# Performance work log

Hardware: AMD Instinct MI355X
Metric: run time of the kernel (lower is better)

Reference implementation:

```python
import jax, jax.numpy as jnp
import numpy as np

N_QUBITS = 11
N_LAYERS = 4
N_FEATURES = 8
N_SAMPLES = 16
MEAS_QUBITS = (0, 1, 2, 3)
DIM = 2 ** N_QUBITS


def _cnot_matrix(control, target, n):
    # Faithful to get_single_CNOT_matrix: qubit 0 is the MOST significant bit
    # (bin(i).zfill(n) indexing). Column i maps to row with target bit flipped
    # when control bit is 1.
    idx = np.arange(2 ** n)
    ctrl = (idx >> (n - 1 - control)) & 1
    rows = np.where(ctrl == 1, idx ^ (1 << (n - 1 - target)), idx)
    u = np.zeros((2 ** n, 2 ** n), np.float32)
    u[rows, idx] = 1.0
    return jnp.asarray(u, jnp.complex64)


def _get_angles(X, weights, biases):
    # X: (B, F) -> angles (B, L, Q, 3), tiling features with repetition
    B, F = X.shape
    n_angles = N_QUBITS * N_LAYERS * 3
    reps = n_angles // F + 1
    Xe = jnp.tile(X, (1, reps))[:, :n_angles].reshape(B, N_LAYERS, N_QUBITS, 3)
    return Xe * weights[None] + biases[None]


def _single_qubit_unitaries(ang):
    # ang: (B, Q, 3) = (phi, theta, omega)  ->  (B, Q, 2, 2) complex Rot gates
    phi, theta, omega = ang[..., 0], ang[..., 1], ang[..., 2]
    ct = jnp.cos(theta / 2)
    st = jnp.sin(theta / 2)
    po = (phi + omega) / 2
    pm = (phi - omega) / 2
    m00 = jnp.exp(-1j * po) * ct
    m01 = -jnp.exp(1j * pm) * st
    m10 = jnp.exp(-1j * pm) * st
    m11 = jnp.exp(1j * po) * ct
    M = jnp.stack([m00, m01, m10, m11], axis=-1)
    return M.reshape(ang.shape[0], ang.shape[1], 2, 2).astype(jnp.complex64)


def _system_unitary(M):
    # Sequential Kronecker product over qubits (qubit 0 = leftmost factor),
    # identical math to the source's einsum-based kron: (B, 2^n, 2^n).
    B = M.shape[0]
    U = M[:, 0]
    for q in range(1, N_QUBITS):
        d = U.shape[1]
        U = (U[:, :, None, :, None] * M[:, q][:, None, :, None, :]).reshape(B, d * 2, d * 2)
    return U


def setup_inputs() -> dict:
    key = jax.random.key(0)
    k1, k2, k3 = jax.random.split(key, 3)
    X = jax.random.normal(k1, (N_SAMPLES, N_FEATURES), jnp.float32)
    weights = jax.random.uniform(k2, (N_LAYERS, N_QUBITS, 3), jnp.float32)
    biases = jax.random.uniform(k3, (N_LAYERS, N_QUBITS, 3), jnp.float32)
    return {"X": X, "weights": weights, "biases": biases}


def reference(X, weights, biases):
    B = X.shape[0]
    angles = _get_angles(X, weights, biases)  # (B, L, Q, 3)
    state = jnp.zeros((B, DIM), jnp.complex64).at[:, 0].set(1.0)
    ring = [(i, i + 1) for i in range(N_QUBITS - 1)] + [(N_QUBITS - 1, 0)]
    cnots = [_cnot_matrix(c, t, N_QUBITS) for c, t in ring]
    for l in range(N_LAYERS):
        U = _system_unitary(_single_qubit_unitaries(angles[:, l]))  # (B, D, D)
        state = jnp.einsum('aij,aj->ai', U, state)
        for Uc in cnots:
            state = jnp.einsum('ij,aj->ai', Uc, state)
    probs = jnp.abs(state) ** 2  # (B, D) float32
    idx = jnp.arange(DIM)
    outs = [jnp.sum(probs * (1.0 - 2.0 * ((idx >> (N_QUBITS - 1 - q)) & 1)).astype(probs.dtype), axis=1)
            for q in MEAS_QUBITS]
    return jnp.stack(outs, axis=1)  # (B, n_meas)
```

## Files before the change

### kernel.cpp

```cpp
#include <hip/hip_runtime.h>

#define NQ 11
#define NL 4
#define NF 8
#define DIM 2048
#define NGATES (NL * NQ)

__host__ __device__ constexpr int ring_perm(int y) {
    int z = y ^ ((y & 1) << 10);
    for (int k = 10; k >= 1; --k)
        z ^= ((z >> (11 - k)) & 1) << (10 - k);
    return z;
}

__device__ __forceinline__ int swz(int i) { return i ^ ((i >> 5) & 31); }

__device__ __forceinline__ void wave_sync() { __builtin_amdgcn_wave_barrier(); }

__device__ __forceinline__ float2 cmul(float2 a, float2 b) {
    return make_float2(a.x * b.x - a.y * b.y, a.x * b.y + a.y * b.x);
}

__device__ __forceinline__ void rot_pair(float2& a, float2& c,
                                         const float4 M0, const float4 M1) {
    float2 na, nc;
    na.x = M0.x * a.x - M0.y * a.y + M0.z * c.x - M0.w * c.y;
    na.y = M0.x * a.y + M0.y * a.x + M0.z * c.y + M0.w * c.x;
    nc.x = M1.x * a.x - M1.y * a.y + M1.z * c.x - M1.w * c.y;
    nc.y = M1.x * a.y + M1.y * a.x + M1.z * c.y + M1.w * c.x;
    a = na; c = nc;
}

template<int P2, int P1, int P0, bool PERM>
__device__ __forceinline__ void group3(const float2* __restrict__ src,
                                       float2* __restrict__ dst,
                                       const float (*gm)[8], int g, int base) {
    constexpr int E2 = 1 << P2, E1 = 1 << P1, E0 = 1 << P0;
    constexpr int K2 = PERM ? ring_perm(1 << P2) : (1 << P2);
    constexpr int K1 = PERM ? ring_perm(1 << P1) : (1 << P1);
    constexpr int K0 = PERM ? ring_perm(1 << P0) : (1 << P0);

    const float4* mA = (const float4*)gm[g];
    const float4* mB = (const float4*)gm[g + 1];
    const float4* mC = (const float4*)gm[g + 2];
    const float4 A0 = mA[0], A1 = mA[1];
    const float4 B0 = mB[0], B1 = mB[1];
    const float4 C0 = mC[0], C1 = mC[1];

    const int rb = PERM ? ring_perm(base) : base;
    float2 s[8];
#pragma unroll
    for (int k = 0; k < 8; ++k) {
        const int idx = rb ^ ((k & 4) ? K2 : 0) ^ ((k & 2) ? K1 : 0) ^ ((k & 1) ? K0 : 0);
        s[k] = src[swz(idx)];
    }
    rot_pair(s[0], s[4], A0, A1); rot_pair(s[1], s[5], A0, A1);
    rot_pair(s[2], s[6], A0, A1); rot_pair(s[3], s[7], A0, A1);
    rot_pair(s[0], s[2], B0, B1); rot_pair(s[1], s[3], B0, B1);
    rot_pair(s[4], s[6], B0, B1); rot_pair(s[5], s[7], B0, B1);
    rot_pair(s[0], s[1], C0, C1); rot_pair(s[2], s[3], C0, C1);
    rot_pair(s[4], s[5], C0, C1); rot_pair(s[6], s[7], C0, C1);
#pragma unroll
    for (int k = 0; k < 8; ++k) {
        const int a = base | ((k & 4) ? E2 : 0) | ((k & 2) ? E1 : 0) | ((k & 1) ? E0 : 0);
        dst[swz(a)] = s[k];
    }
}

__device__ __forceinline__ void group2q(float2* buf, const float (*gm)[8],
                                        int g, int t) {
    const float4* mB = (const float4*)gm[g];
    const float4* mC = (const float4*)gm[g + 1];
    const float4 B0 = mB[0], B1 = mB[1];
    const float4 C0 = mC[0], C1 = mC[1];
#pragma unroll
    for (int j = 0; j < 2; ++j) {
        const int base = (t << 3) | (j << 2);
        float2 s[4];
#pragma unroll
        for (int k = 0; k < 4; ++k) s[k] = buf[swz(base | k)];
        rot_pair(s[0], s[2], B0, B1); rot_pair(s[1], s[3], B0, B1);
        rot_pair(s[0], s[1], C0, C1); rot_pair(s[2], s[3], C0, C1);
#pragma unroll
        for (int k = 0; k < 4; ++k) buf[swz(base | k)] = s[k];
    }
}

__global__ __launch_bounds__(256)
void qsim_kernel(const float* __restrict__ X, const float* __restrict__ W,
                 const float* __restrict__ Bi, float* __restrict__ out)
{
    __shared__ float2 bufA[DIM];
    __shared__ float2 bufB[DIM];
    __shared__ __align__(16) float gm[NGATES][8];
    __shared__ float sc[3 * NGATES][2];
    __shared__ float red[4][4];

    const int b = blockIdx.x;
    const int t = threadIdx.x;

    if (t < 3 * NGATES) {
        const int g = t / 3, c = t - 3 * g;
        const int base = g * 3;
        const float x0 = X[b * NF + ((base + 0) & 7)];
        const float x1 = X[b * NF + ((base + 1) & 7)];
        const float x2 = X[b * NF + ((base + 2) & 7)];
        const float phi   = x0 * W[base + 0] + Bi[base + 0];
        const float theta = x1 * W[base + 1] + Bi[base + 1];
        const float omega = x2 * W[base + 2] + Bi[base + 2];
        const float arg = (c == 0) ? 0.5f * theta
                        : (c == 1) ? 0.5f * (phi + omega)
                                   : 0.5f * (phi - omega);
        float s_, c_; sincosf(arg, &s_, &c_);
        sc[t][0] = s_; sc[t][1] = c_;
    }
    __syncthreads();
    if (t < NGATES) {
        const float sh  = sc[3 * t][0],     ch  = sc[3 * t][1];
        const float spo = sc[3 * t + 1][0], cpo = sc[3 * t + 1][1];
        const float spm = sc[3 * t + 2][0], cpm = sc[3 * t + 2][1];
        gm[t][0] =  cpo * ch;  gm[t][1] = -spo * ch;
        gm[t][2] = -cpm * sh;  gm[t][3] = -spm * sh;
        gm[t][4] =  cpm * sh;  gm[t][5] = -spm * sh;
        gm[t][6] =  cpo * ch;  gm[t][7] =  spo * ch;
    }
    __syncthreads();

    float2* S = bufA;
    float2* T = bufB;

    {
        float2 c0[11], c1[11];
#pragma unroll
        for (int q = 0; q < 11; ++q) {
            c0[q] = make_float2(gm[q][0], gm[q][1]);
            c1[q] = make_float2(gm[q][4], gm[q][5]);
        }
        float2 P = ((t >> 0) & 1) ? c1[10] : c0[10];
#pragma unroll
        for (int bbit = 1; bbit < 8; ++bbit)
            P = cmul(P, ((t >> bbit) & 1) ? c1[10 - bbit] : c0[10 - bbit]);
        float2 t2[4];
        t2[0] = cmul(c0[1], c0[0]);
        t2[1] = cmul(c1[1], c0[0]);
        t2[2] = cmul(c0[1], c1[0]);
        t2[3] = cmul(c1[1], c1[0]);
#pragma unroll
        for (int k = 0; k < 8; ++k) {
            const float2 h = cmul((k & 1) ? c1[2] : c0[2], t2[k >> 1]);
            S[swz(t + 256 * k)] = cmul(P, h);
        }
    }
    __syncthreads();

    for (int l = 1; l < NL; ++l) {
        group3<10, 9, 8, true>(S, T, gm, l * NQ + 0, t); { float2* x = S; S = T; T = x; }
        __syncthreads();
        const int base765 = ((t >> 5) << 8) | (t & 31);
        const int base432 = ((t >> 2) << 5) | (t & 3);
        group3<7, 6, 5, false>(S, S, gm, l * NQ + 3, base765);  wave_sync();
        group3<4, 3, 2, false>(S, S, gm, l * NQ + 6, base432);  wave_sync();
        group2q(S, gm, l * NQ + 9, t);
        __syncthreads();
    }

    const int rp_t = ring_perm(t);
    float v[4] = {0.f, 0.f, 0.f, 0.f};
#pragma unroll
    for (int k = 0; k < 8; ++k) {
        const int src = rp_t ^ ((k & 4) ? ring_perm(1 << 10) : 0)
                             ^ ((k & 2) ? ring_perm(1 << 9)  : 0)
                             ^ ((k & 1) ? ring_perm(1 << 8)  : 0);
        const float2 a = S[swz(src)];
        const float p = a.x * a.x + a.y * a.y;
        v[0] += (k & 4) ? -p : p;
        v[1] += (k & 2) ? -p : p;
        v[2] += (k & 1) ? -p : p;
        v[3] += (t & 128) ? -p : p;
    }
#pragma unroll
    for (int q = 0; q < 4; ++q)
#pragma unroll
        for (int off = 32; off >= 1; off >>= 1)
            v[q] += __shfl_down(v[q], off, 64);
    if ((t & 63) == 0) {
#pragma unroll
        for (int q = 0; q < 4; ++q) red[t >> 6][q] = v[q];
    }
    __syncthreads();
    if (t < 4) {
        out[b * 4 + t] = red[0][t] + red[1][t] + red[2][t] + red[3][t];
    }
}

extern "C" void kernel_launch(void* const* d_in, const int* in_sizes, int n_in,
                              void* d_out, int out_size, void* d_ws, size_t ws_size,
                              hipStream_t stream) {
    const float* X  = (const float*)d_in[0];
    const float* W  = (const float*)d_in[1];
    const float* Bi = (const float*)d_in[2];
    float* out = (float*)d_out;
    qsim_kernel<<<16, 256, 0, stream>>>(X, W, Bi, out);
}
```

Measured before the change: 66.44 us.

## Fuse final gate layer with measurement and use per-wave gate setup sync

The last layer's final two rotations are fused with the PauliZ measurement: each thread computes probabilities in registers and derives the parity signs through the ring CNOT permutation, which removes one block barrier and a shared-memory pass. Gate-matrix setup is restructured so each wave handles whole gates, letting a wave barrier replace a block barrier. The layer loop is also unrolled. This relies on correct parity-mask algebra for the CNOT ring.

Result: faster. 65.05 us (median of 2 runs) (-2.1%).

```diff
diff --git a/kernel.cpp b/kernel.cpp
--- a/kernel.cpp
+++ b/kernel.cpp
@@ -86,6 +86,40 @@
     }
 }
 
+__device__ __forceinline__ void group2q_meas(const float2* __restrict__ buf,
+                                             const float (*gm)[8], int g, int t,
+                                             float v[4]) {
+    const float4* mB = (const float4*)gm[g];
+    const float4* mC = (const float4*)gm[g + 1];
+    const float4 B0 = mB[0], B1 = mB[1];
+    const float4 C0 = mC[0], C1 = mC[1];
+    const int tb = t << 3;
+    const int p0 = __popc(tb & 0x3FF) & 1;
+    const int p1 = __popc(tb & 0x600) & 1;
+    const int p2 = __popc(tb & 0x700) & 1;
+    const int p3 = __popc(tb & 0x780) & 1;
+    float Psum = 0.f, Aalt = 0.f;
+#pragma unroll
+    for (int j = 0; j < 2; ++j) {
+        const int base = tb | (j << 2);
+        float2 s[4];
+#pragma unroll
+        for (int k = 0; k < 4; ++k) s[k] = buf[swz(base | k)];
+        rot_pair(s[0], s[2], B0, B1); rot_pair(s[1], s[3], B0, B1);
+        rot_pair(s[0], s[1], C0, C1); rot_pair(s[2], s[3], C0, C1);
+#pragma unroll
+        for (int k = 0; k < 4; ++k) {
+            const float p = s[k].x * s[k].x + s[k].y * s[k].y;
+            Psum += p;
+            Aalt += (__popc((j << 2) | k) & 1) ? -p : p;
+        }
+    }
+    v[0] = p0 ? -Aalt : Aalt;
+    v[1] = p1 ? -Psum : Psum;
+    v[2] = p2 ? -Psum : Psum;
+    v[3] = p3 ? -Psum : Psum;
+}
+
 __global__ __launch_bounds__(256)
 void qsim_kernel(const float* __restrict__ X, const float* __restrict__ W,
                  const float* __restrict__ Bi, float* __restrict__ out)
@@ -93,36 +127,40 @@
     __shared__ float2 bufA[DIM];
     __shared__ float2 bufB[DIM];
     __shared__ __align__(16) float gm[NGATES][8];
-    __shared__ float sc[3 * NGATES][2];
+    __shared__ float sc[192][2];
     __shared__ float red[4][4];
 
     const int b = blockIdx.x;
     const int t = threadIdx.x;
 
-    if (t < 3 * NGATES) {
-        const int g = t / 3, c = t - 3 * g;
-        const int base = g * 3;
-        const float x0 = X[b * NF + ((base + 0) & 7)];
-        const float x1 = X[b * NF + ((base + 1) & 7)];
-        const float x2 = X[b * NF + ((base + 2) & 7)];
-        const float phi   = x0 * W[base + 0] + Bi[base + 0];
-        const float theta = x1 * W[base + 1] + Bi[base + 1];
-        const float omega = x2 * W[base + 2] + Bi[base + 2];
-        const float arg = (c == 0) ? 0.5f * theta
-                        : (c == 1) ? 0.5f * (phi + omega)
-                                   : 0.5f * (phi - omega);
-        float s_, c_; sincosf(arg, &s_, &c_);
-        sc[t][0] = s_; sc[t][1] = c_;
-    }
-    __syncthreads();
-    if (t < NGATES) {
-        const float sh  = sc[3 * t][0],     ch  = sc[3 * t][1];
-        const float spo = sc[3 * t + 1][0], cpo = sc[3 * t + 1][1];
-        const float spm = sc[3 * t + 2][0], cpm = sc[3 * t + 2][1];
-        gm[t][0] =  cpo * ch;  gm[t][1] = -spo * ch;
-        gm[t][2] = -cpm * sh;  gm[t][3] = -spm * sh;
-        gm[t][4] =  cpm * sh;  gm[t][5] = -spm * sh;
-        gm[t][6] =  cpo * ch;  gm[t][7] =  spo * ch;
+    {
+        const int sl = t & 63;
+        const int g = 21 * (t >> 6) + sl / 3;
+        const int c = sl % 3;
+        if (sl < 63 && g < NGATES) {
+            const int base = g * 3;
+            const float x0 = X[b * NF + ((base + 0) & 7)];
+            const float x1 = X[b * NF + ((base + 1) & 7)];
+            const float x2 = X[b * NF + ((base + 2) & 7)];
+            const float phi   = x0 * W[base + 0] + Bi[base + 0];
+            const float theta = x1 * W[base + 1] + Bi[base + 1];
+            const float omega = x2 * W[base + 2] + Bi[base + 2];
+            const float arg = (c == 0) ? 0.5f * theta
+                            : (c == 1) ? 0.5f * (phi + omega)
+                                       : 0.5f * (phi - omega);
+            float s_, c_; sincosf(arg, &s_, &c_);
+            sc[t][0] = s_; sc[t][1] = c_;
+        }
+        wave_sync();
+        if (sl < 63 && g < NGATES && c == 0) {
+            const float sh  = sc[t][0],     ch  = sc[t][1];
+            const float spo = sc[t + 1][0], cpo = sc[t + 1][1];
+            const float spm = sc[t + 2][0], cpm = sc[t + 2][1];
+            gm[g][0] =  cpo * ch;  gm[g][1] = -spo * ch;
+            gm[g][2] = -cpm * sh;  gm[g][3] = -spm * sh;
+            gm[g][4] =  cpm * sh;  gm[g][5] = -spm * sh;
+            gm[g][6] =  cpo * ch;  gm[g][7] =  spo * ch;
+        }
     }
     __syncthreads();
 
@@ -153,6 +191,7 @@
     }
     __syncthreads();
 
+#pragma unroll
     for (int l = 1; l < NL; ++l) {
         group3<10, 9, 8, true>(S, T, gm, l * NQ + 0, t); { float2* x = S; S = T; T = x; }
         __syncthreads();
@@ -160,24 +199,15 @@
         const int base432 = ((t >> 2) << 5) | (t & 3);
         group3<7, 6, 5, false>(S, S, gm, l * NQ + 3, base765);  wave_sync();
         group3<4, 3, 2, false>(S, S, gm, l * NQ + 6, base432);  wave_sync();
-        group2q(S, gm, l * NQ + 9, t);
-        __syncthreads();
-    }
-
-    const int rp_t = ring_perm(t);
-    float v[4] = {0.f, 0.f, 0.f, 0.f};
-#pragma unroll
-    for (int k = 0; k < 8; ++k) {
-        const int src = rp_t ^ ((k & 4) ? ring_perm(1 << 10) : 0)
-                             ^ ((k & 2) ? ring_perm(1 << 9)  : 0)
-                             ^ ((k & 1) ? ring_perm(1 << 8)  : 0);
-        const float2 a = S[swz(src)];
-        const float p = a.x * a.x + a.y * a.y;
-        v[0] += (k & 4) ? -p : p;
-        v[1] += (k & 2) ? -p : p;
-        v[2] += (k & 1) ? -p : p;
-        v[3] += (t & 128) ? -p : p;
-    }
+        if (l < NL - 1) {
+            group2q(S, gm, l * NQ + 9, t);
+            __syncthreads();
+        }
+    }
+
+    float v[4];
+    group2q_meas(S, gm, (NL - 1) * NQ + 9, t, v);
+
 #pragma unroll
     for (int q = 0; q < 4; ++q)
 #pragma unroll
```
